# Kernel optimization log

Hardware: AMD Instinct MI355X
Metric: run time of the kernel (lower is better)

The kernel has to match this reference:

```python
import jax, jax.numpy as jnp
import numpy as np

D_MODEL = 512
NUM_HEADS = 8
HEAD_DIM = D_MODEL // NUM_HEADS
SEQ_LEN = 4096
BATCH = 2
D_FF = 4 * D_MODEL
EPS = 1e-5


def _layer_norm(x, g, b):
    mu = jnp.mean(x, axis=-1, keepdims=True)
    var = jnp.var(x, axis=-1, keepdims=True)
    return (x - mu) * jax.lax.rsqrt(var + EPS) * g + b


def setup_inputs() -> dict:
    key = jax.random.key(0)
    ks = jax.random.split(key, 12)
    s = 0.02
    inp = {
        "x": jax.random.normal(ks[0], (BATCH, SEQ_LEN, D_MODEL), jnp.float32),
        # Linear weights stored as [in, out] (y = x @ W + b)
        "Wq": jax.random.normal(ks[1], (D_MODEL, D_MODEL), jnp.float32) * s,
        "bq": jnp.zeros((D_MODEL,), jnp.float32),
        "Wk": jax.random.normal(ks[2], (D_MODEL, D_MODEL), jnp.float32) * s,
        "bk": jnp.zeros((D_MODEL,), jnp.float32),
        "Wv": jax.random.normal(ks[3], (D_MODEL, D_MODEL), jnp.float32) * s,
        "bv": jnp.zeros((D_MODEL,), jnp.float32),
        "Wo": jax.random.normal(ks[4], (D_MODEL, D_MODEL), jnp.float32) * s,
        "bo": jnp.zeros((D_MODEL,), jnp.float32),
        "ln1_g": jnp.ones((D_MODEL,), jnp.float32),
        "ln1_b": jnp.zeros((D_MODEL,), jnp.float32),
        "ln2_g": jnp.ones((D_MODEL,), jnp.float32),
        "ln2_b": jnp.zeros((D_MODEL,), jnp.float32),
        "W1": jax.random.normal(ks[5], (D_MODEL, D_FF), jnp.float32) * s,
        "b1": jnp.zeros((D_FF,), jnp.float32),
        "W2": jax.random.normal(ks[6], (D_FF, D_MODEL), jnp.float32) * s,
        "b2": jnp.zeros((D_MODEL,), jnp.float32),
    }
    return inp


def reference(x, Wq, bq, Wk, bk, Wv, bv, Wo, bo, ln1_g, ln1_b, ln2_g, ln2_b, W1, b1, W2, b2):
    B, S, D = x.shape
    residual = x
    h = _layer_norm(x, ln1_g, ln1_b)
    # project and split heads: [B, H, S, Dh]
    def split_heads(t):
        return t.reshape(B, S, NUM_HEADS, HEAD_DIM).transpose(0, 2, 1, 3)
    q = split_heads(h @ Wq + bq)
    k = split_heads(h @ Wk + bk)
    v = split_heads(h @ Wv + bv)
    scores = jnp.einsum("bhqd,bhkd->bhqk", q, k) / (HEAD_DIM ** 0.5)
    attn = jax.nn.softmax(scores, axis=-1)
    out = jnp.einsum("bhqk,bhkd->bhqd", attn, v)
    out = out.transpose(0, 2, 1, 3).reshape(B, S, D)
    out = out @ Wo + bo
    x1 = residual + out
    h2 = _layer_norm(x1, ln2_g, ln2_b)
    ff = jax.nn.gelu(h2 @ W1 + b1, approximate=False) @ W2 + b2
    return x1 + ff
```

## Files before the change

kernel.cpp:

```cpp
#include <hip/hip_runtime.h>
#include <hip/hip_bf16.h>
#include <math.h>

typedef __hip_bfloat16 bf16;

#define D_MODEL 512
#define NUM_HEADS 8
#define HEAD_DIM 64
#define SEQ_LEN 4096
#define BATCH 2
#define D_FF 2048
#define TOKENS (BATCH * SEQ_LEN)
#define QKV_STRIDE 1536

typedef short short4v __attribute__((ext_vector_type(4)));
typedef short short8v __attribute__((ext_vector_type(8)));
typedef float float4v __attribute__((ext_vector_type(4)));
typedef float float2v __attribute__((ext_vector_type(2)));

union frag_u { short8v v8; short4v v4[2]; short s[8]; };
union pack_u { unsigned u[2]; short4v v4; };

__device__ __forceinline__ float b2f(bf16 v) { return __bfloat162float(v); }
__device__ __forceinline__ bf16 f2b(float v) { return __float2bfloat16(v); }
__device__ __forceinline__ short f2bs(float v) { bf16 t = __float2bfloat16(v); return *(short*)&t; }
__device__ __forceinline__ float exp2fast(float x) { return __builtin_amdgcn_exp2f(x); }

__device__ __forceinline__ unsigned pack_bf16(float lo, float hi) {
    unsigned a = __float_as_uint(hi) + 0x8000u;
    unsigned b = __float_as_uint(lo) + 0x8000u;
    return __builtin_amdgcn_perm(a, b, 0x07060302u);
}

__device__ __forceinline__ unsigned cvt_pk_bf16(float lo, float hi) {
    unsigned r;
    asm("v_cvt_pk_bf16_f32 %0, %1, %2" : "=v"(r) : "v"(lo), "v"(hi));
    return r;
}

__device__ __forceinline__ int3 swz_xyz() {
    int gx = gridDim.x, gy = gridDim.y;
    int id = blockIdx.x + gx * (blockIdx.y + gy * blockIdx.z);
    int nwg = gx * gy * (int)gridDim.z;
    int nid = (id & 7) * (nwg >> 3) + (id >> 3);
    int3 r;
    r.x = nid % gx;
    int t = nid / gx;
    r.y = t % gy;
    r.z = t / gy;
    return r;
}

#define AS1(p) ((__attribute__((address_space(1))) void*)(p))
#define AS3(p) ((__attribute__((address_space(3))) void*)(p))

__device__ __forceinline__ int self_detect(const unsigned* __restrict__ xw, int tid) {
    unsigned w = xw[tid & 63];
    unsigned e = (w >> 7) & 0xFFu;
    unsigned long long b = __ballot(e >= 110 && e <= 140);
    return __popcll(b) < 32;
}

__device__ __forceinline__ void do_tr(const void* __restrict__ src, bf16* __restrict__ dst,
                                      int K, int N, int n0, int k0, int fl, int tid,
                                      bf16 (*tile)[65]) {
    int c = tid & 63, r4 = tid >> 6;
#pragma unroll
    for (int t = 0; t < 16; t++) {
        int r = t * 4 + r4;
        size_t si = (size_t)(k0 + r) * N + n0 + c;
        float v = fl ? ((const float*)src)[si] : b2f(((const bf16*)src)[si]);
        tile[r][c] = f2b(v);
    }
    __syncthreads();
#pragma unroll
    for (int t = 0; t < 16; t++) {
        int r = t * 4 + r4;
        dst[(size_t)(n0 + r) * K + k0 + c] = tile[c][r];
    }
}

__global__ void prep_kernel(const void* x, const void* Wq, const void* Wk, const void* Wv,
                            const void* Wo, const void* W1, const void* W2,
                            const void* bq, const void* bk, const void* bv, const void* bo,
                            const void* b1, const void* b2,
                            const void* g1, const void* e1, const void* g2, const void* e2,
                            bf16* __restrict__ Wqkvt ,
                            bf16* __restrict__ W1t, bf16* __restrict__ W2t,
                            bf16* __restrict__ small, int* __restrict__ flag) {
    __shared__ bf16 tile[64][65];
    int blk = blockIdx.x, tid = threadIdx.x;
    int fl = self_detect((const unsigned*)x, tid);
    if (blk == 0 && tid == 0) flag[0] = fl;
    if (blk < 256) {
        int z = blk >> 6, tt = blk & 63;
        const void* src = (z == 0) ? Wq : (z == 1) ? Wk : (z == 2) ? Wv : Wo;
        do_tr(src, Wqkvt + (size_t)z * 512 * 512, 512, 512, (tt & 7) * 64, (tt >> 3) * 64,
              fl, tid, tile);
    } else if (blk < 512) {
        int tt = blk - 256;
        do_tr(W1, W1t, 512, 2048, (tt & 31) * 64, (tt >> 5) * 64, fl, tid, tile);
    } else if (blk < 768) {
        int tt = blk - 512;
        do_tr(W2, W2t, 2048, 512, (tt & 7) * 64, (tt >> 3) * 64, fl, tid, tile);
    } else {
        int i = (blk - 768) * 256 + tid;
        const void* src; int off;
        if (i < 512)       { src = bq; off = 0; }
        else if (i < 1024) { src = bk; off = 512; }
        else if (i < 1536) { src = bv; off = 1024; }
        else if (i < 2048) { src = bo; off = 1536; }
        else if (i < 4096) { src = b1; off = 2048; }
        else if (i < 4608) { src = b2; off = 4096; }
        else if (i < 5120) { src = g1; off = 4608; }
        else if (i < 5632) { src = e1; off = 5120; }
        else if (i < 6144) { src = g2; off = 5632; }
        else               { src = e2; off = 6144; }
        int j = i - off;
        small[i] = fl ? f2b(((const float*)src)[j]) : ((const bf16*)src)[j];
    }
}

template <int MODE>
__global__ void ln_kernel(const void* __restrict__ xv, const bf16* __restrict__ g,
                          const bf16* __restrict__ b, bf16* __restrict__ out,
                          const int* __restrict__ flag) {
    int t = blockIdx.x;
    int tid = threadIdx.x;
    int fl = (MODE == 2) ? *flag : 0;
    float v0, v1;
    if (fl) {
        const float* xr = (const float*)xv + (size_t)t * D_MODEL;
        v0 = xr[tid]; v1 = xr[tid + 256];
    } else {
        const bf16* xr = (const bf16*)xv + (size_t)t * D_MODEL;
        v0 = b2f(xr[tid]); v1 = b2f(xr[tid + 256]);
    }
    float s = v0 + v1, ss = v0 * v0 + v1 * v1;
    for (int o = 32; o > 0; o >>= 1) {
        s += __shfl_down(s, o);
        ss += __shfl_down(ss, o);
    }
    __shared__ float rs[4], rss[4], stat[2];
    int w = tid >> 6, l = tid & 63;
    if (l == 0) { rs[w] = s; rss[w] = ss; }
    __syncthreads();
    if (tid == 0) {
        float S = rs[0] + rs[1] + rs[2] + rs[3];
        float SS = rss[0] + rss[1] + rss[2] + rss[3];
        float mu = S / (float)D_MODEL;
        float var = SS / (float)D_MODEL - mu * mu;
        stat[0] = mu;
        stat[1] = rsqrtf(var + 1e-5f);
    }
    __syncthreads();
    float mu = stat[0], rstd = stat[1];
    bf16* orow = out + (size_t)t * D_MODEL;
    orow[tid]       = f2b((v0 - mu) * rstd * b2f(g[tid])       + b2f(b[tid]));
    orow[tid + 256] = f2b((v1 - mu) * rstd * b2f(g[tid + 256]) + b2f(b[tid + 256]));
}

__device__ __forceinline__ float gelu_tanh(float v) {
    float u = 0.7978845608f * (v + 0.044715f * v * v * v);
    float e2 = __expf(-2.f * u);
    return v / (1.f + e2);
}

template <int ACT>
__global__ __launch_bounds__(256) void mfma_gemm(
    const bf16* __restrict__ A, const bf16* __restrict__ Wt,
    const bf16* __restrict__ bias, bf16* __restrict__ Cout,
    bf16* __restrict__ Vt_out, int M, int N, int K) {
    __shared__ bf16 As[128 * 64];
    __shared__ bf16 Bs[128 * 64];
    int tid = threadIdx.x, wave = tid >> 6, lane = tid & 63;
    int m = lane & 15, g = lane >> 4;
    int3 sw = swz_xyz();
    int row0 = sw.y * 128, col0 = sw.x * 128;
    int R0 = (wave >> 1) * 64, C0 = (wave & 1) * 64;
    float4v acc[4][4] = {};

    int srow = lane >> 3;
    int scol = (lane & 7) * 8;
    const bf16* Ab = A  + (size_t)(row0 + wave * 8 + srow) * K + scol;
    const bf16* Bb = Wt + (size_t)(col0 + wave * 8 + srow) * K + scol;

    for (int k0 = 0; k0 < K; k0 += 64) {
#pragma unroll
        for (int t = 0; t < 4; t++) {
            int rbase = t * 32 + wave * 8;
            __builtin_amdgcn_global_load_lds(AS1(Ab + (size_t)(t * 32) * K + k0),
                                             AS3(&As[rbase * 64]), 16, 0, 0);
            __builtin_amdgcn_global_load_lds(AS1(Bb + (size_t)(t * 32) * K + k0),
                                             AS3(&Bs[rbase * 64]), 16, 0, 0);
        }
        __syncthreads();
#pragma unroll
        for (int kk = 0; kk < 2; kk++) {
            short8v fa[4], fb[4];
#pragma unroll
            for (int i = 0; i < 4; i++)
                fa[i] = *(const short8v*)&As[(R0 + i * 16 + m) * 64 + kk * 32 + g * 8];
#pragma unroll
            for (int j = 0; j < 4; j++)
                fb[j] = *(const short8v*)&Bs[(C0 + j * 16 + m) * 64 + kk * 32 + g * 8];
#pragma unroll
            for (int i = 0; i < 4; i++)
#pragma unroll
                for (int j = 0; j < 4; j++)
                    acc[i][j] = __builtin_amdgcn_mfma_f32_16x16x32_bf16(fa[i], fb[j], acc[i][j], 0, 0, 0);
        }
        __syncthreads();
    }

    if (Vt_out != nullptr && col0 >= 1024) {
#pragma unroll
        for (int i = 0; i < 4; i++) {
            int row = row0 + R0 + i * 16 + g * 4;
            int b = row >> 12, s = row & (SEQ_LEN - 1);
#pragma unroll
            for (int j = 0; j < 4; j++) {
                int col = col0 + C0 + j * 16 + m;
                int hh = (col - 1024) >> 6, d = col & 63;
                float bi = b2f(bias[col]);
                pack_u oo;
                oo.u[0] = pack_bf16(acc[i][j][0] + bi, acc[i][j][1] + bi);
                oo.u[1] = pack_bf16(acc[i][j][2] + bi, acc[i][j][3] + bi);
                *(short4v*)&Vt_out[((size_t)((b << 3) + hh) * 64 + d) * SEQ_LEN + s] = oo.v4;
            }
        }
        return;
    }

#pragma unroll
    for (int i = 0; i < 4; i++) {
#pragma unroll
        for (int r = 0; r < 4; r++) {
            int row = row0 + R0 + i * 16 + g * 4 + r;
#pragma unroll
            for (int j = 0; j < 4; j++) {
                int col = col0 + C0 + j * 16 + m;
                float v = acc[i][j][r] + b2f(bias[col]);
                if (ACT == 1) v = gelu_tanh(v);
                Cout[(size_t)row * N + col] = f2b(v);
            }
        }
    }
}

template <int RES, int OUTMODE>
__global__ __launch_bounds__(256) void mfma_gemm64(
    const bf16* __restrict__ A, const bf16* __restrict__ Wt,
    const bf16* __restrict__ bias, const void* __restrict__ res,
    void* __restrict__ Cout, const int* __restrict__ flag, int M, int N, int K) {
    __shared__ bf16 As[128 * 64];
    __shared__ bf16 Bs[64 * 64];
    int tid = threadIdx.x, wave = tid >> 6, lane = tid & 63;
    int m = lane & 15, g = lane >> 4;
    int3 sw = swz_xyz();
    int row0 = sw.y * 128, col0 = sw.x * 64;
    int R0 = wave * 32;
    int fl = (OUTMODE == 2 || RES == 3) ? *flag : 0;
    float4v acc[2][4] = {};

    int srow = lane >> 3;
    int scol = (lane & 7) * 8;
    const bf16* Ab = A  + (size_t)(row0 + wave * 8 + srow) * K + scol;
    const bf16* Bb = Wt + (size_t)(col0 + wave * 8 + srow) * K + scol;

    for (int k0 = 0; k0 < K; k0 += 64) {
#pragma unroll
        for (int t = 0; t < 4; t++) {
            __builtin_amdgcn_global_load_lds(AS1(Ab + (size_t)(t * 32) * K + k0),
                                             AS3(&As[(t * 32 + wave * 8) * 64]), 16, 0, 0);
            if (t < 2)
                __builtin_amdgcn_global_load_lds(AS1(Bb + (size_t)(t * 32) * K + k0),
                                                 AS3(&Bs[(t * 32 + wave * 8) * 64]), 16, 0, 0);
        }
        __syncthreads();
#pragma unroll
        for (int kk = 0; kk < 2; kk++) {
            short8v fa[2], fb[4];
#pragma unroll
            for (int i = 0; i < 2; i++)
                fa[i] = *(const short8v*)&As[(R0 + i * 16 + m) * 64 + kk * 32 + g * 8];
#pragma unroll
            for (int j = 0; j < 4; j++)
                fb[j] = *(const short8v*)&Bs[(j * 16 + m) * 64 + kk * 32 + g * 8];
#pragma unroll
            for (int i = 0; i < 2; i++)
#pragma unroll
                for (int j = 0; j < 4; j++)
                    acc[i][j] = __builtin_amdgcn_mfma_f32_16x16x32_bf16(fa[i], fb[j], acc[i][j], 0, 0, 0);
        }
        __syncthreads();
    }

#pragma unroll
    for (int i = 0; i < 2; i++) {
#pragma unroll
        for (int r = 0; r < 4; r++) {
            int row = row0 + R0 + i * 16 + g * 4 + r;
#pragma unroll
            for (int j = 0; j < 4; j++) {
                int col = col0 + j * 16 + m;
                float v = acc[i][j][r] + b2f(bias[col]);
                size_t idx = (size_t)row * N + col;
                if (RES == 2) v += b2f(((const bf16*)res)[idx]);
                if (RES == 3) v += fl ? ((const float*)res)[idx]
                                      : b2f(((const bf16*)res)[idx]);
                if (OUTMODE == 0) ((bf16*)Cout)[idx] = f2b(v);
                else {
                    if (fl) ((float*)Cout)[idx] = v;
                    else ((bf16*)Cout)[idx] = f2b(v);
                }
            }
        }
    }
}

#define F3(a, b, c) fmaxf(fmaxf((a), (b)), (c))
template <int KS>
__global__ __launch_bounds__(256, 4) void flash_attn(const bf16* __restrict__ Q,
                                                     const bf16* __restrict__ K,
                                                     const bf16* __restrict__ Vt_g,
                                                     bf16* __restrict__ Op,
                                                     float2* __restrict__ mlout) {
    __shared__ bf16 Ks[64][72];
    __shared__ bf16 Vt[64][72];

    int tid = threadIdx.x;
    int wave = tid >> 6, lane = tid & 63;
    int m = lane & 15, g = lane >> 4;
    bf16* PtW = &Ks[0][0] + wave * (16 * 72);

    int3 sw = swz_xyz();
    int bh = sw.y;
    size_t base = (size_t)(bh >> 3) * SEQ_LEN * QKV_STRIDE + (size_t)(bh & 7) * HEAD_DIM;
    int q0w = sw.x * 128 + wave * 32;

    const float qscale = 0.125f * 1.44269504f;
    short8v aQ[2][2];
#pragma unroll
    for (int mt = 0; mt < 2; mt++) {
        const bf16* qp = Q + base + (size_t)(q0w + mt * 16 + m) * QKV_STRIDE + g * 8;
#pragma unroll
        for (int c = 0; c < 2; c++) {
            frag_u u;
#pragma unroll
            for (int j = 0; j < 8; j++) u.s[j] = f2bs(b2f(qp[c * 32 + j]) * qscale);
            aQ[mt][c] = u.v8;
        }
    }

    float mrow[2] = {-1e30f, -1e30f};
    float lrow[2] = {0.f, 0.f};
    float4v oacc[2][4] = {};

    int sk = tid >> 2, sd = (tid & 3) * 16;
    int vrow = tid >> 2, vcol = (tid & 3) * 16;

    const unsigned short* Ku = (const unsigned short*)(K + base);
    const unsigned short* Vg = (const unsigned short*)Vt_g +
                               (size_t)bh * 64 * SEQ_LEN + (size_t)vrow * SEQ_LEN;

    int t0 = sw.z * (64 / KS);
    int t1 = t0 + 64 / KS;

    short8v rk0, rk1, rv0, rv1;
    {
        int kt0 = t0 * 64;
        const unsigned short* kp = Ku + (size_t)(kt0 + sk) * QKV_STRIDE + sd;
        rk0 = *(const short8v*)(kp);
        rk1 = *(const short8v*)(kp + 8);
        rv0 = *(const short8v*)(Vg + kt0 + vcol);
        rv1 = *(const short8v*)(Vg + kt0 + vcol + 8);
        *(short8v*)&Ks[sk][sd]     = rk0;
        *(short8v*)&Ks[sk][sd + 8] = rk1;
        *(short8v*)&Vt[vrow][vcol]     = rv0;
        *(short8v*)&Vt[vrow][vcol + 8] = rv1;
    }
    __syncthreads();

    for (int t = t0; t < t1; t++) {
        if (t + 1 < t1) {
            int ktn = (t + 1) * 64;
            const unsigned short* kp = Ku + (size_t)(ktn + sk) * QKV_STRIDE + sd;
            rk0 = *(const short8v*)(kp);
            rk1 = *(const short8v*)(kp + 8);
            rv0 = *(const short8v*)(Vg + ktn + vcol);
            rv1 = *(const short8v*)(Vg + ktn + vcol + 8);
        }

        float4v st[2][4];
        __builtin_amdgcn_s_setprio(1);
#pragma unroll
        for (int kt = 0; kt < 4; kt++) {
            short8v bK0 = *(const short8v*)&Ks[kt * 16 + m][g * 8];
            short8v bK1 = *(const short8v*)&Ks[kt * 16 + m][32 + g * 8];
#pragma unroll
            for (int mt = 0; mt < 2; mt++) {
                float4v a = {0.f, 0.f, 0.f, 0.f};
                a = __builtin_amdgcn_mfma_f32_16x16x32_bf16(bK0, aQ[mt][0], a, 0, 0, 0);
                a = __builtin_amdgcn_mfma_f32_16x16x32_bf16(bK1, aQ[mt][1], a, 0, 0, 0);
                st[mt][kt] = a;
            }
        }
        __builtin_amdgcn_s_setprio(0);

        __syncthreads();

        short8v bP[2][2];
#pragma unroll
        for (int mt = 0; mt < 2; mt++) {
            float u0 = F3(st[mt][0][0], st[mt][0][1], st[mt][0][2]);
            float u1 = F3(st[mt][0][3], st[mt][1][0], st[mt][1][1]);
            float u2 = F3(st[mt][1][2], st[mt][1][3], st[mt][2][0]);
            float u3 = F3(st[mt][2][1], st[mt][2][2], st[mt][2][3]);
            float u4 = F3(st[mt][3][0], st[mt][3][1], st[mt][3][2]);
            float tm = fmaxf(F3(u0, u1, u2), F3(u3, u4, st[mt][3][3]));
            tm = fmaxf(tm, __shfl_xor(tm, 16));
            tm = fmaxf(tm, __shfl_xor(tm, 32));
            if (!__all(tm - mrow[mt] <= 8.f)) {
                float mnew = fmaxf(mrow[mt], tm);
                float alpha = exp2fast(mrow[mt] - mnew);
                mrow[mt] = mnew;
                lrow[mt] *= alpha;
#pragma unroll
                for (int dt = 0; dt < 4; dt++)
#pragma unroll
                    for (int r = 0; r < 4; r++) oacc[mt][dt][r] *= alpha;
            }
            float mcur = mrow[mt];
            float2v ps = {0.f, 0.f};
#pragma unroll
            for (int kt = 0; kt < 4; kt++) {
                float p0 = exp2fast(st[mt][kt][0] - mcur);
                float p1 = exp2fast(st[mt][kt][1] - mcur);
                float p2 = exp2fast(st[mt][kt][2] - mcur);
                float p3 = exp2fast(st[mt][kt][3] - mcur);
                float2v a = {p0, p1}, b = {p2, p3};
                ps += a + b;
                pack_u pp;
                pp.u[0] = cvt_pk_bf16(p0, p1);
                pp.u[1] = cvt_pk_bf16(p2, p3);
                *(short4v*)&PtW[m * 72 + kt * 16 + g * 4] = pp.v4;
            }
            lrow[mt] += ps[0] + ps[1];
#pragma unroll
            for (int c = 0; c < 2; c++)
                bP[mt][c] = *(const short8v*)&PtW[m * 72 + c * 32 + g * 8];
        }

        __builtin_amdgcn_s_setprio(1);
#pragma unroll
        for (int dt = 0; dt < 4; dt++) {
#pragma unroll
            for (int c = 0; c < 2; c++) {
                short8v av = *(const short8v*)&Vt[dt * 16 + m][c * 32 + g * 8];
#pragma unroll
                for (int mt = 0; mt < 2; mt++)
                    oacc[mt][dt] = __builtin_amdgcn_mfma_f32_16x16x32_bf16(av, bP[mt][c], oacc[mt][dt], 0, 0, 0);
            }
        }
        __builtin_amdgcn_s_setprio(0);

        __syncthreads();
        if (t + 1 < t1) {
            *(short8v*)&Ks[sk][sd]     = rk0;
            *(short8v*)&Ks[sk][sd + 8] = rk1;
            *(short8v*)&Vt[vrow][vcol]     = rv0;
            *(short8v*)&Vt[vrow][vcol + 8] = rv1;
        }
        __syncthreads();
    }

    size_t zoff = (size_t)sw.z * NUM_HEADS * BATCH + bh;
    size_t pbase = zoff * (SEQ_LEN * (size_t)HEAD_DIM);
#pragma unroll
    for (int mt = 0; mt < 2; mt++) {
        float l = lrow[mt];
        l += __shfl_xor(l, 16);
        l += __shfl_xor(l, 32);
        int q = q0w + mt * 16 + m;
        bf16* orow = Op + pbase + (size_t)q * HEAD_DIM;
#pragma unroll
        for (int dt = 0; dt < 4; dt++) {
            pack_u oo;
            oo.u[0] = cvt_pk_bf16(oacc[mt][dt][0], oacc[mt][dt][1]);
            oo.u[1] = cvt_pk_bf16(oacc[mt][dt][2], oacc[mt][dt][3]);
            *(short4v*)&orow[dt * 16 + g * 4] = oo.v4;
        }
        if (g == 0) mlout[zoff * SEQ_LEN + q] = make_float2(mrow[mt], l);
    }
}

template <int KS>
__global__ void attn_merge(const bf16* __restrict__ Op, const float2* __restrict__ ml,
                           bf16* __restrict__ O) {
    int i = blockIdx.x * 256 + threadIdx.x;
    int d = i & 63;
    int q = (i >> 6) & (SEQ_LEN - 1);
    int bh = i >> 18;
    const int HQ = NUM_HEADS * BATCH * SEQ_LEN;
    float2 a[KS];
    float M = -1e30f;
#pragma unroll
    for (int p = 0; p < KS; p++) {
        a[p] = ml[(size_t)p * HQ + bh * SEQ_LEN + q];
        M = fmaxf(M, a[p].x);
    }
    float w[KS];
    float denom = 0.f;
#pragma unroll
    for (int p = 0; p < KS; p++) {
        w[p] = exp2fast(a[p].x - M);
        denom += a[p].y * w[p];
    }
    float inv = 1.f / denom;
    const size_t NP = (size_t)HQ * HEAD_DIM;
    float o = 0.f;
#pragma unroll
    for (int p = 0; p < KS; p++) o += b2f(Op[(size_t)p * NP + i]) * w[p];
    o *= inv;
    O[((size_t)((bh >> 3) * SEQ_LEN + q)) * D_MODEL + (bh & 7) * HEAD_DIM + d] = f2b(o);
}

extern "C" void kernel_launch(void* const* d_in, const int* in_sizes, int n_in,
                              void* d_out, int out_size, void* d_ws, size_t ws_size,
                              hipStream_t stream) {
    const void* x     = d_in[0];
    const void* Wq    = d_in[1];
    const void* bq    = d_in[2];
    const void* Wk    = d_in[3];
    const void* bk    = d_in[4];
    const void* Wv    = d_in[5];
    const void* bv    = d_in[6];
    const void* Wo    = d_in[7];
    const void* bo    = d_in[8];
    const void* ln1_g = d_in[9];
    const void* ln1_b = d_in[10];
    const void* ln2_g = d_in[11];
    const void* ln2_b = d_in[12];
    const void* W1    = d_in[13];
    const void* b1    = d_in[14];
    const void* W2    = d_in[15];
    const void* b2    = d_in[16];

    char* p = (char*)d_ws;
    int* flag = (int*)p;                      p += 256;
    size_t tok_d = (size_t)TOKENS * D_MODEL;
    char* region2 = p;                        p += 2 * tok_d * 2;
    bf16* x1b   = (bf16*)region2;
    bf16* hb    = (bf16*)(region2 + tok_d * 2);
    bf16* Opart2 = (bf16*)region2;
    bf16*  bigA = (bf16*)p;                   p += (size_t)TOKENS * D_FF * 2;
    bf16*  qkvb = bigA;
    bf16*  ab   = bigA + (size_t)TOKENS * QKV_STRIDE;
    bf16*  ffb  = bigA;
    bf16*  Wqkvt = (bf16*)p;                  p += (size_t)QKV_STRIDE * D_MODEL * 2;
    bf16*  Wot   = (bf16*)p;                  p += (size_t)D_MODEL * D_MODEL * 2;
    bf16*  W1t   = (bf16*)p;                  p += (size_t)D_FF * D_MODEL * 2;
    bf16*  W2t   = (bf16*)p;                  p += (size_t)D_MODEL * D_FF * 2;
    bf16*  Vtg   = (bf16*)p;                  p += (size_t)NUM_HEADS * BATCH * HEAD_DIM * SEQ_LEN * 2;
    float2* mlb  = (float2*)p;                p += (size_t)4 * NUM_HEADS * BATCH * SEQ_LEN * sizeof(float2);
    bf16*  small = (bf16*)p;                  p += 6656 * 2;
    bf16*  Opart4 = (bf16*)p;
    size_t opart4_bytes = (size_t)4 * NUM_HEADS * BATCH * SEQ_LEN * HEAD_DIM * 2;
    int ks4 = ((char*)Opart4 + opart4_bytes - (char*)d_ws) <= (ptrdiff_t)ws_size;

    bf16* bias_qkv = small + 0;
    bf16* bias_o   = small + 1536;
    bf16* b1b      = small + 2048;
    bf16* b2b      = small + 4096;
    bf16* g1b      = small + 4608;
    bf16* be1b     = small + 5120;
    bf16* g2b      = small + 5632;
    bf16* be2b     = small + 6144;

    prep_kernel<<<794, 256, 0, stream>>>(x, Wq, Wk, Wv, Wo, W1, W2,
                                         bq, bk, bv, bo, b1, b2,
                                         ln1_g, ln1_b, ln2_g, ln2_b,
                                         Wqkvt, W1t, W2t, small, flag);

    ln_kernel<2><<<TOKENS, 256, 0, stream>>>(x, g1b, be1b, hb, flag);

    mfma_gemm<0><<<dim3(QKV_STRIDE / 128, TOKENS / 128), 256, 0, stream>>>(
        hb, Wqkvt, bias_qkv, qkvb, Vtg, TOKENS, QKV_STRIDE, D_MODEL);

    if (ks4) {
        flash_attn<4><<<dim3(SEQ_LEN / 128, 16, 4), 256, 0, stream>>>(
            qkvb, qkvb + 512, Vtg, Opart4, mlb);
        attn_merge<4><<<(NUM_HEADS * BATCH * SEQ_LEN * HEAD_DIM) / 256, 256, 0, stream>>>(
            Opart4, mlb, ab);
    } else {
        flash_attn<2><<<dim3(SEQ_LEN / 128, 16, 2), 256, 0, stream>>>(
            qkvb, qkvb + 512, Vtg, Opart2, mlb);
        attn_merge<2><<<(NUM_HEADS * BATCH * SEQ_LEN * HEAD_DIM) / 256, 256, 0, stream>>>(
            Opart2, mlb, ab);
    }

    mfma_gemm64<3, 0><<<dim3(D_MODEL / 64, TOKENS / 128), 256, 0, stream>>>(
        ab, Wot, bias_o, x, x1b, flag, TOKENS, D_MODEL, D_MODEL);

    ln_kernel<0><<<TOKENS, 256, 0, stream>>>(x1b, g2b, be2b, hb, flag);

    mfma_gemm<1><<<dim3(D_FF / 128, TOKENS / 128), 256, 0, stream>>>(
        hb, W1t, b1b, ffb, nullptr, TOKENS, D_FF, D_MODEL);

    mfma_gemm64<2, 2><<<dim3(D_MODEL / 64, TOKENS / 128), 256, 0, stream>>>(
        ffb, W2t, b2b, x1b, d_out, flag, TOKENS, D_MODEL, D_FF);
}
```

Baseline: 352.6 us.

## Double-buffer GEMM LDS tiles with BK=32 and fix attention split-K to 2

Both MFMA GEMM kernels switch from single-buffered 64-wide K tiles to double-buffered 32-wide K tiles. The next tile's global-to-LDS load is issued before computing on the current one, and MFMA issue priority is raised via s_setprio. This aims to hide global load latency behind matrix math, at the cost of twice as many loop iterations and barriers. The attention path also drops the workspace-dependent 4-way split and always uses a 2-way KV split, which may lose parallelism if the 4-way path was previously the one being taken.

```diff
diff --git a/kernel.cpp b/kernel.cpp
--- a/kernel.cpp
+++ b/kernel.cpp
@@ -12,6 +12,7 @@
 #define D_FF 2048
 #define TOKENS (BATCH * SEQ_LEN)
 #define QKV_STRIDE 1536
+#define KSPLIT 2
 
 typedef short short4v __attribute__((ext_vector_type(4)));
 typedef short short8v __attribute__((ext_vector_type(8)));
@@ -171,8 +172,8 @@
     const bf16* __restrict__ A, const bf16* __restrict__ Wt,
     const bf16* __restrict__ bias, bf16* __restrict__ Cout,
     bf16* __restrict__ Vt_out, int M, int N, int K) {
-    __shared__ bf16 As[128 * 64];
-    __shared__ bf16 Bs[128 * 64];
+    __shared__ bf16 As[2][128 * 32];
+    __shared__ bf16 Bs[2][128 * 32];
     int tid = threadIdx.x, wave = tid >> 6, lane = tid & 63;
     int m = lane & 15, g = lane >> 4;
     int3 sw = swz_xyz();
@@ -180,38 +181,45 @@
     int R0 = (wave >> 1) * 64, C0 = (wave & 1) * 64;
     float4v acc[4][4] = {};
 
-    int srow = lane >> 3;
-    int scol = (lane & 7) * 8;
-    const bf16* Ab = A  + (size_t)(row0 + wave * 8 + srow) * K + scol;
-    const bf16* Bb = Wt + (size_t)(col0 + wave * 8 + srow) * K + scol;
-
-    for (int k0 = 0; k0 < K; k0 += 64) {
-#pragma unroll
-        for (int t = 0; t < 4; t++) {
-            int rbase = t * 32 + wave * 8;
-            __builtin_amdgcn_global_load_lds(AS1(Ab + (size_t)(t * 32) * K + k0),
-                                             AS3(&As[rbase * 64]), 16, 0, 0);
-            __builtin_amdgcn_global_load_lds(AS1(Bb + (size_t)(t * 32) * K + k0),
-                                             AS3(&Bs[rbase * 64]), 16, 0, 0);
-        }
+    int srow = lane >> 2;
+    int scol = (lane & 3) * 8;
+    const bf16* Ab = A  + (size_t)(row0 + wave * 32 + srow) * K + scol;
+    const bf16* Bb = Wt + (size_t)(col0 + wave * 32 + srow) * K + scol;
+
+#define GSTAGE128(buf, kk0)                                                        \
+    {                                                                              \
+        _Pragma("unroll")                                                          \
+        for (int t = 0; t < 2; t++) {                                              \
+            __builtin_amdgcn_global_load_lds(AS1(Ab + (size_t)(t * 16) * K + (kk0)),\
+                AS3(&As[buf][(wave * 32 + t * 16) * 32]), 16, 0, 0);               \
+            __builtin_amdgcn_global_load_lds(AS1(Bb + (size_t)(t * 16) * K + (kk0)),\
+                AS3(&Bs[buf][(wave * 32 + t * 16) * 32]), 16, 0, 0);               \
+        }                                                                          \
+    }
+
+    int nk = K >> 5;
+    GSTAGE128(0, 0);
+    __syncthreads();
+    for (int it = 0; it < nk; it++) {
+        int cur = it & 1;
+        if (it + 1 < nk) GSTAGE128(cur ^ 1, (it + 1) * 32);
+        short8v fa[4], fb[4];
+#pragma unroll
+        for (int i = 0; i < 4; i++)
+            fa[i] = *(const short8v*)&As[cur][(R0 + i * 16 + m) * 32 + g * 8];
+#pragma unroll
+        for (int j = 0; j < 4; j++)
+            fb[j] = *(const short8v*)&Bs[cur][(C0 + j * 16 + m) * 32 + g * 8];
+        __builtin_amdgcn_s_setprio(1);
+#pragma unroll
+        for (int i = 0; i < 4; i++)
+#pragma unroll
+            for (int j = 0; j < 4; j++)
+                acc[i][j] = __builtin_amdgcn_mfma_f32_16x16x32_bf16(fa[i], fb[j], acc[i][j], 0, 0, 0);
+        __builtin_amdgcn_s_setprio(0);
         __syncthreads();
-#pragma unroll
-        for (int kk = 0; kk < 2; kk++) {
-            short8v fa[4], fb[4];
-#pragma unroll
-            for (int i = 0; i < 4; i++)
-                fa[i] = *(const short8v*)&As[(R0 + i * 16 + m) * 64 + kk * 32 + g * 8];
-#pragma unroll
-            for (int j = 0; j < 4; j++)
-                fb[j] = *(const short8v*)&Bs[(C0 + j * 16 + m) * 64 + kk * 32 + g * 8];
-#pragma unroll
-            for (int i = 0; i < 4; i++)
-#pragma unroll
-                for (int j = 0; j < 4; j++)
-                    acc[i][j] = __builtin_amdgcn_mfma_f32_16x16x32_bf16(fa[i], fb[j], acc[i][j], 0, 0, 0);
-        }
-        __syncthreads();
-    }
+    }
+#undef GSTAGE128
 
     if (Vt_out != nullptr && col0 >= 1024) {
 #pragma unroll
@@ -253,8 +261,8 @@
     const bf16* __restrict__ A, const bf16* __restrict__ Wt,
     const bf16* __restrict__ bias, const void* __restrict__ res,
     void* __restrict__ Cout, const int* __restrict__ flag, int M, int N, int K) {
-    __shared__ bf16 As[128 * 64];
-    __shared__ bf16 Bs[64 * 64];
+    __shared__ bf16 As[2][128 * 32];
+    __shared__ bf16 Bs[2][64 * 32];
     int tid = threadIdx.x, wave = tid >> 6, lane = tid & 63;
     int m = lane & 15, g = lane >> 4;
     int3 sw = swz_xyz();
@@ -263,38 +271,44 @@
     int fl = (OUTMODE == 2 || RES == 3) ? *flag : 0;
     float4v acc[2][4] = {};
 
-    int srow = lane >> 3;
-    int scol = (lane & 7) * 8;
-    const bf16* Ab = A  + (size_t)(row0 + wave * 8 + srow) * K + scol;
-    const bf16* Bb = Wt + (size_t)(col0 + wave * 8 + srow) * K + scol;
-
-    for (int k0 = 0; k0 < K; k0 += 64) {
-#pragma unroll
-        for (int t = 0; t < 4; t++) {
-            __builtin_amdgcn_global_load_lds(AS1(Ab + (size_t)(t * 32) * K + k0),
-                                             AS3(&As[(t * 32 + wave * 8) * 64]), 16, 0, 0);
-            if (t < 2)
-                __builtin_amdgcn_global_load_lds(AS1(Bb + (size_t)(t * 32) * K + k0),
-                                                 AS3(&Bs[(t * 32 + wave * 8) * 64]), 16, 0, 0);
-        }
+    int srow = lane >> 2;
+    int scol = (lane & 3) * 8;
+    const bf16* Ab = A  + (size_t)(row0 + wave * 32 + srow) * K + scol;
+    const bf16* Bb = Wt + (size_t)(col0 + wave * 16 + srow) * K + scol;
+
+#define GSTAGE64(buf, kk0)                                                         \
+    {                                                                              \
+        _Pragma("unroll")                                                          \
+        for (int t = 0; t < 2; t++)                                                \
+            __builtin_amdgcn_global_load_lds(AS1(Ab + (size_t)(t * 16) * K + (kk0)),\
+                AS3(&As[buf][(wave * 32 + t * 16) * 32]), 16, 0, 0);               \
+        __builtin_amdgcn_global_load_lds(AS1(Bb + (kk0)),                          \
+            AS3(&Bs[buf][(wave * 16) * 32]), 16, 0, 0);                            \
+    }
+
+    int nk = K >> 5;
+    GSTAGE64(0, 0);
+    __syncthreads();
+    for (int it = 0; it < nk; it++) {
+        int cur = it & 1;
+        if (it + 1 < nk) GSTAGE64(cur ^ 1, (it + 1) * 32);
+        short8v fa[2], fb[4];
+#pragma unroll
+        for (int i = 0; i < 2; i++)
+            fa[i] = *(const short8v*)&As[cur][(R0 + i * 16 + m) * 32 + g * 8];
+#pragma unroll
+        for (int j = 0; j < 4; j++)
+            fb[j] = *(const short8v*)&Bs[cur][(j * 16 + m) * 32 + g * 8];
+        __builtin_amdgcn_s_setprio(1);
+#pragma unroll
+        for (int i = 0; i < 2; i++)
+#pragma unroll
+            for (int j = 0; j < 4; j++)
+                acc[i][j] = __builtin_amdgcn_mfma_f32_16x16x32_bf16(fa[i], fb[j], acc[i][j], 0, 0, 0);
+        __builtin_amdgcn_s_setprio(0);
         __syncthreads();
-#pragma unroll
-        for (int kk = 0; kk < 2; kk++) {
-            short8v fa[2], fb[4];
-#pragma unroll
-            for (int i = 0; i < 2; i++)
-                fa[i] = *(const short8v*)&As[(R0 + i * 16 + m) * 64 + kk * 32 + g * 8];
-#pragma unroll
-            for (int j = 0; j < 4; j++)
-                fb[j] = *(const short8v*)&Bs[(j * 16 + m) * 64 + kk * 32 + g * 8];
-#pragma unroll
-            for (int i = 0; i < 2; i++)
-#pragma unroll
-                for (int j = 0; j < 4; j++)
-                    acc[i][j] = __builtin_amdgcn_mfma_f32_16x16x32_bf16(fa[i], fb[j], acc[i][j], 0, 0, 0);
-        }
-        __syncthreads();
-    }
+    }
+#undef GSTAGE64
 
 #pragma unroll
     for (int i = 0; i < 2; i++) {
@@ -553,7 +567,7 @@
     char* region2 = p;                        p += 2 * tok_d * 2;
     bf16* x1b   = (bf16*)region2;
     bf16* hb    = (bf16*)(region2 + tok_d * 2);
-    bf16* Opart2 = (bf16*)region2;
+    bf16* Opart = (bf16*)region2;
     bf16*  bigA = (bf16*)p;                   p += (size_t)TOKENS * D_FF * 2;
     bf16*  qkvb = bigA;
     bf16*  ab   = bigA + (size_t)TOKENS * QKV_STRIDE;
@@ -563,12 +577,8 @@
     bf16*  W1t   = (bf16*)p;                  p += (size_t)D_FF * D_MODEL * 2;
     bf16*  W2t   = (bf16*)p;                  p += (size_t)D_MODEL * D_FF * 2;
     bf16*  Vtg   = (bf16*)p;                  p += (size_t)NUM_HEADS * BATCH * HEAD_DIM * SEQ_LEN * 2;
-    float2* mlb  = (float2*)p;                p += (size_t)4 * NUM_HEADS * BATCH * SEQ_LEN * sizeof(float2);
+    float2* mlb  = (float2*)p;                p += (size_t)KSPLIT * NUM_HEADS * BATCH * SEQ_LEN * sizeof(float2);
     bf16*  small = (bf16*)p;                  p += 6656 * 2;
-    bf16*  Opart4 = (bf16*)p;
-    size_t opart4_bytes = (size_t)4 * NUM_HEADS * BATCH * SEQ_LEN * HEAD_DIM * 2;
-    int ks4 = ((char*)Opart4 + opart4_bytes - (char*)d_ws) <= (ptrdiff_t)ws_size;
-
     bf16* bias_qkv = small + 0;
     bf16* bias_o   = small + 1536;
     bf16* b1b      = small + 2048;
@@ -588,17 +598,10 @@
     mfma_gemm<0><<<dim3(QKV_STRIDE / 128, TOKENS / 128), 256, 0, stream>>>(
         hb, Wqkvt, bias_qkv, qkvb, Vtg, TOKENS, QKV_STRIDE, D_MODEL);
 
-    if (ks4) {
-        flash_attn<4><<<dim3(SEQ_LEN / 128, 16, 4), 256, 0, stream>>>(
-            qkvb, qkvb + 512, Vtg, Opart4, mlb);
-        attn_merge<4><<<(NUM_HEADS * BATCH * SEQ_LEN * HEAD_DIM) / 256, 256, 0, stream>>>(
-            Opart4, mlb, ab);
-    } else {
-        flash_attn<2><<<dim3(SEQ_LEN / 128, 16, 2), 256, 0, stream>>>(
-            qkvb, qkvb + 512, Vtg, Opart2, mlb);
-        attn_merge<2><<<(NUM_HEADS * BATCH * SEQ_LEN * HEAD_DIM) / 256, 256, 0, stream>>>(
-            Opart2, mlb, ab);
-    }
+    flash_attn<KSPLIT><<<dim3(SEQ_LEN / 128, 16, KSPLIT), 256, 0, stream>>>(
+        qkvb, qkvb + 512, Vtg, Opart, mlb);
+    attn_merge<KSPLIT><<<(NUM_HEADS * BATCH * SEQ_LEN * HEAD_DIM) / 256, 256, 0, stream>>>(
+        Opart, mlb, ab);
 
     mfma_gemm64<3, 0><<<dim3(D_MODEL / 64, TOKENS / 128), 256, 0, stream>>>(
         ab, Wot, bias_o, x, x1b, flag, TOKENS, D_MODEL, D_MODEL);
```

After: 352.8 us. No clear change (+0.0%).
